# Kernel tuning notes

Hardware: AMD Instinct MI355X
Metric: run time of the kernel (lower is better)

Reference implementation:

```python
import jax, jax.numpy as jnp
import numpy as np

B, N = 2, 8192
D_POINTS, D_MODEL, K = 64, 128, 16


def _lin(key, fi, fo):
    return jax.random.normal(key, (fi, fo), jnp.float32) / np.sqrt(fi)


def setup_inputs() -> dict:
    key = jax.random.key(0)
    ks = jax.random.split(key, 16)
    return {
        "xyz": jax.random.normal(ks[0], (B, N, 3), jnp.float32),
        "normals": jax.random.normal(ks[1], (B, N, 3), jnp.float32),
        "features": jax.random.normal(ks[2], (B, N, D_POINTS), jnp.float32),
        "fc1_w": _lin(ks[3], D_POINTS, D_MODEL), "fc1_b": jnp.zeros((D_MODEL,), jnp.float32),
        "fc2_w": _lin(ks[4], D_MODEL, D_POINTS), "fc2_b": jnp.zeros((D_POINTS,), jnp.float32),
        "gamma_w1": _lin(ks[5], D_MODEL, D_MODEL), "gamma_b1": jnp.zeros((D_MODEL,), jnp.float32),
        "gamma_w2": _lin(ks[6], D_MODEL, D_MODEL), "gamma_b2": jnp.zeros((D_MODEL,), jnp.float32),
        "delta_w1": _lin(ks[7], 3, D_MODEL), "delta_b1": jnp.zeros((D_MODEL,), jnp.float32),
        "delta_w2": _lin(ks[8], D_MODEL, D_MODEL), "delta_b2": jnp.zeros((D_MODEL,), jnp.float32),
        "wq": _lin(ks[9], D_MODEL, D_MODEL),
        "wk": _lin(ks[10], D_MODEL, D_MODEL),
        "wv": _lin(ks[11], D_MODEL, D_MODEL),
    }


def _gather(points, idx):
    # points: (b, n, c), idx: (b, n, k) -> (b, n, k, c)
    b, n, c = points.shape
    k = idx.shape[-1]
    flat = jnp.take_along_axis(points, idx.reshape(b, n * k, 1), axis=1)
    return flat.reshape(b, n, k, c)


def reference(xyz, normals, features, fc1_w, fc1_b, fc2_w, fc2_b,
              gamma_w1, gamma_b1, gamma_w2, gamma_b2,
              delta_w1, delta_b1, delta_w2, delta_b2, wq, wk, wv):
    # pairwise squared distances (b, n, n)
    sq = jnp.sum(xyz * xyz, axis=-1)
    dists = sq[:, :, None] + sq[:, None, :] - 2.0 * jnp.einsum('bnd,bmd->bnm', xyz, xyz)
    _, knn_idx = jax.lax.top_k(-dists, K)  # k smallest distances (includes self)

    knn_xyz = _gather(xyz, knn_idx)                      # (b, n, k, 3)
    x = features @ fc1_w + fc1_b                         # (b, n, d_model)
    q = x @ wq                                           # (b, n, d_model)
    k_nbr = _gather(x @ wk, knn_idx)                     # (b, n, k, d_model)
    v_nbr = _gather(x @ wv, knn_idx)                     # (b, n, k, d_model)

    # positional encoding: fc_delta(rel_pos), ends with ReLU
    rel = xyz[:, :, None, :] - knn_xyz                   # (b, n, k, 3)
    pos_enc = jax.nn.relu(jax.nn.relu(rel @ delta_w1 + delta_b1) @ delta_w2 + delta_b2)

    # vector attention logits: fc_gamma(q - k + pos_enc)
    h = q[:, :, None, :] - k_nbr + pos_enc
    logits = jax.nn.relu(h @ gamma_w1 + gamma_b1) @ gamma_w2 + gamma_b2
    attn = jax.nn.softmax(logits / np.sqrt(D_MODEL), axis=-2)  # softmax over neighbors

    res = jnp.einsum('bnkf,bnkf->bnf', attn, v_nbr + pos_enc)
    res = res @ fc2_w + fc2_b + features
    return res, attn
```

## Files before the change

### kernel.cpp

```cpp
#include <hip/hip_runtime.h>
#include <cstdint>

typedef unsigned long long ull;
typedef __bf16 bf16x8 __attribute__((ext_vector_type(8)));
typedef float f32x4 __attribute__((ext_vector_type(4)));
typedef float f32x2 __attribute__((ext_vector_type(2)));

#define NPTS 8192
#define NB 2
#define KNN 16
#define DM 128
#define PADK 136
#define PADF 72

__device__ __forceinline__ float sq3f(float x, float y, float z) {
    return __fadd_rn(__fadd_rn(__fmul_rn(x, x), __fmul_rn(y, y)), __fmul_rn(z, z));
}
__device__ __forceinline__ unsigned ford(unsigned u) {
    return (u & 0x80000000u) ? ~u : (u | 0x80000000u);
}
__device__ __forceinline__ float inv_ford(unsigned f) {
    unsigned u = (f & 0x80000000u) ? (f ^ 0x80000000u) : ~f;
    return __uint_as_float(u);
}
__device__ __forceinline__ f32x2 pk_mul(f32x2 a, f32x2 b) {
    f32x2 d;
    asm("v_pk_mul_f32 %0, %1, %2" : "=v"(d) : "v"(a), "v"(b));
    return d;
}
__device__ __forceinline__ f32x2 pk_add(f32x2 a, f32x2 b) {
    f32x2 d;
    asm("v_pk_add_f32 %0, %1, %2" : "=v"(d) : "v"(a), "v"(b));
    return d;
}

__device__ __forceinline__ void knn_body(const float* __restrict__ xyz,
                                         int* __restrict__ idx_out,
                                         char* lds, int bid) {
    float4* xsA = (float4*)lds;
    float4* xsB = (float4*)(lds + 8192);
    const int t = threadIdx.x;
    const int wv = t >> 6, lane = t & 63;
    const int q_id = bid * 4 + wv;
    const int b = q_id >> 13;
    const int i = q_id & (NPTS - 1);
    const float* xb = xyz + (size_t)b * NPTS * 3;
    const float qx = xb[3 * i + 0], qy = xb[3 * i + 1], qz = xb[3 * i + 2];
    const float sqi = sq3f(qx, qy, qz);
    const f32x2 qx2 = {qx, qx}, qy2 = {qy, qy}, qz2 = {qz, qz};
    const f32x2 sqi2 = {sqi, sqi}, ntwo2 = {-2.0f, -2.0f};

    unsigned list_hi = 0xffffffffu, list_lo = 0xffffffffu;
    float thrF = __uint_as_float(0x7f800000u);

#define INSERT(FC, CKLO)                                                                 \
    {                                                                                    \
        unsigned ck_hi = ford(__float_as_uint(FC));                                      \
        unsigned ck_lo = (CKLO);                                                         \
        unsigned ph = __shfl_up(list_hi, 1);                                             \
        unsigned pl = __shfl_up(list_lo, 1);                                             \
        bool lt = (ck_hi < list_hi) || (ck_hi == list_hi && ck_lo < list_lo);            \
        bool ge = (lane == 0) || (ck_hi > ph) || (ck_hi == ph && ck_lo >= pl);           \
        list_hi = lt ? (ge ? ck_hi : ph) : list_hi;                                      \
        list_lo = lt ? (ge ? ck_lo : pl) : list_lo;                                      \
        unsigned th = (unsigned)__builtin_amdgcn_readlane((int)list_hi, 15);             \
        th = (th > 0xff800000u) ? 0xff800000u : th;            \
        thrF = fminf(thrF, inv_ford(th));                                                \
    }

    for (int ch = 0; ch < 8; ++ch) {
        __syncthreads();
#pragma unroll
        for (int e = 0; e < 2; e++) {
            int s = t + e * 256;
            int c0 = ((s >> 6) << 7) + (s & 63);
            int g = ch * 1024 + c0;
            float x0 = xb[3 * g + 0], y0 = xb[3 * g + 1], z0 = xb[3 * g + 2];
            float x1 = xb[3 * (g + 64) + 0], y1 = xb[3 * (g + 64) + 1], z1 = xb[3 * (g + 64) + 2];
            xsA[s] = make_float4(x0, x1, y0, y1);
            xsB[s] = make_float4(z0, z1, sq3f(x0, y0, z0), sq3f(x1, y1, z1));
        }
        __syncthreads();
        for (int m = 0; m < 8; m++) {
            const int s = m * 64 + lane;
            float4 A = xsA[s];
            float4 B = xsB[s];
            f32x2 ax = {A.x, A.y}, ay = {A.z, A.w};
            f32x2 bz = {B.x, B.y}, bs = {B.z, B.w};
            f32x2 p1 = pk_mul(qx2, ax);
            f32x2 p2 = pk_mul(qy2, ay);
            f32x2 p3 = pk_mul(qz2, bz);
            f32x2 s1 = pk_add(p1, p2);
            f32x2 s2 = pk_add(s1, p3);
            f32x2 num = pk_add(sqi2, bs);
            f32x2 tm = pk_mul(ntwo2, s2);
            f32x2 dd = pk_add(num, tm);
            float dA = dd.x, dB = dd.y;
            if (ch == 0 && m == 0) {
                float mn = fminf(dA, dB);
                mn = fminf(mn, __shfl_xor(mn, 1));
                mn = fminf(mn, __shfl_xor(mn, 2));
                float mx = mn;
                mx = fmaxf(mx, __shfl_xor(mx, 4));
                mx = fmaxf(mx, __shfl_xor(mx, 8));
                mx = fmaxf(mx, __shfl_xor(mx, 16));
                mx = fmaxf(mx, __shfl_xor(mx, 32));
                thrF = mx;
            }
            ull balA = __ballot(dA <= thrF);
            ull balB = __ballot(dB <= thrF);
            if ((balA | balB) == 0ull) continue;
            const unsigned jbase = (unsigned)(ch * 1024 + m * 128);
            while (balA) {
                int l = (int)__builtin_ctzll(balA);
                balA &= balA - 1;
                float fc = __uint_as_float(
                    (unsigned)__builtin_amdgcn_readlane(__float_as_int(dA), l));
                if (fc <= thrF) INSERT(fc, jbase + (unsigned)l)
            }
            while (balB) {
                int l = (int)__builtin_ctzll(balB);
                balB &= balB - 1;
                float fc = __uint_as_float(
                    (unsigned)__builtin_amdgcn_readlane(__float_as_int(dB), l));
                if (fc <= thrF) INSERT(fc, jbase + 64u + (unsigned)l)
            }
        }
    }
#undef INSERT
    if (lane < 16)
        idx_out[q_id * 16 + lane] = (int)list_lo;
}

__device__ __forceinline__ void xqkv_body(const float* __restrict__ feats,
                                          const __bf16* __restrict__ fc1t,
                                          const float* __restrict__ fc1_b,
                                          const __bf16* __restrict__ wqt,
                                          const __bf16* __restrict__ wkt,
                                          const __bf16* __restrict__ wvt,
                                          float* __restrict__ qo,
                                          float* __restrict__ kko,
                                          float* __restrict__ vvo,
                                          char* lds, int bid) {
    __bf16* Af = (__bf16*)lds;
    __bf16* Ab = (__bf16*)(lds + 9216);
    const int t = threadIdx.x;
    const int base = bid * 64;

#pragma unroll
    for (int e = 0; e < 4; e++) {
        int id = t + e * 256;
        int r = id >> 4, c4 = id & 15;
        float4 v = *(const float4*)&feats[(size_t)(base + r) * 64 + c4 * 4];
        __bf16* d = &Af[r * PADF + c4 * 4];
        d[0] = (__bf16)v.x; d[1] = (__bf16)v.y; d[2] = (__bf16)v.z; d[3] = (__bf16)v.w;
    }
    __syncthreads();

    const int lane = t & 63;
    const int lr = lane & 15, lg = lane >> 4;
    const int rb = (t >> 6) * 16;

    f32x4 xacc[8];
#pragma unroll
    for (int ct = 0; ct < 8; ct++) {
        float bb = fc1_b[ct * 16 + lr];
        xacc[ct] = (f32x4){bb, bb, bb, bb};
    }
#pragma unroll
    for (int kt = 0; kt < 2; kt++) {
        const int ko = kt * 32 + 8 * lg;
        bf16x8 a0 = *(const bf16x8*)&Af[(rb + lr) * PADF + ko];
#pragma unroll
        for (int ct = 0; ct < 8; ct++) {
            bf16x8 bv = *(const bf16x8*)&fc1t[(ct * 16 + lr) * 64 + ko];
            xacc[ct] = __builtin_amdgcn_mfma_f32_16x16x32_bf16(a0, bv, xacc[ct], 0, 0, 0);
        }
    }
#pragma unroll
    for (int ct = 0; ct < 8; ct++)
#pragma unroll
        for (int e = 0; e < 4; e++)
            Ab[(rb + 4 * lg + e) * PADK + ct * 16 + lr] = (__bf16)xacc[ct][e];

#define QGEMM(WPTR, OUT)                                                                   \
    {                                                                                      \
        f32x4 accg[8];                                                                     \
        _Pragma("unroll")                                                                  \
        for (int ct = 0; ct < 8; ct++) accg[ct] = (f32x4){0.f, 0.f, 0.f, 0.f};             \
        _Pragma("unroll")                                                                  \
        for (int kt = 0; kt < 4; kt++) {                                                   \
            const int ko = kt * 32 + 8 * lg;                                               \
            bf16x8 a0 = *(const bf16x8*)&Ab[(rb + lr) * PADK + ko];                        \
            _Pragma("unroll")                                                              \
            for (int ct = 0; ct < 8; ct++) {                                               \
                bf16x8 bv = *(const bf16x8*)&WPTR[(ct * 16 + lr) * 128 + ko];              \
                accg[ct] = __builtin_amdgcn_mfma_f32_16x16x32_bf16(a0, bv, accg[ct], 0, 0, 0); \
            }                                                                              \
        }                                                                                  \
        _Pragma("unroll")                                                                  \
        for (int ct = 0; ct < 8; ct++)                                                     \
            _Pragma("unroll")                                                              \
            for (int e = 0; e < 4; e++)                                                    \
                OUT[(size_t)(base + rb + 4 * lg + e) * 128 + ct * 16 + lr] = accg[ct][e];  \
    }

    QGEMM(wqt, qo)
    QGEMM(wkt, kko)
    QGEMM(wvt, vvo)
#undef QGEMM
}

__global__ __launch_bounds__(256, 6) void mega_kernel(const float* __restrict__ xyz,
                                                      int* __restrict__ idxw,
                                                      const float* __restrict__ feats,
                                                      const __bf16* __restrict__ fc1t,
                                                      const float* __restrict__ fc1_b,
                                                      const __bf16* __restrict__ wqt,
                                                      const __bf16* __restrict__ wkt,
                                                      const __bf16* __restrict__ wvt,
                                                      float* __restrict__ qo,
                                                      float* __restrict__ kko,
                                                      float* __restrict__ vvo) {
    __shared__ __align__(16) char lds[26624];
    const int g = blockIdx.x / 17;
    const int p = blockIdx.x % 17;
    if (p == 0)
        xqkv_body(feats, fc1t, fc1_b, wqt, wkt, wvt, qo, kko, vvo, lds, g);
    else
        knn_body(xyz, idxw, lds, g * 16 + (p - 1));
}

__global__ __launch_bounds__(256) void wprep_kernel(const float* __restrict__ d2,
                                                    const float* __restrict__ g1,
                                                    const float* __restrict__ g2,
                                                    const float* __restrict__ wq,
                                                    const float* __restrict__ wk,
                                                    const float* __restrict__ wv,
                                                    const float* __restrict__ fc1,
                                                    __bf16* __restrict__ d2t,
                                                    __bf16* __restrict__ g1t,
                                                    __bf16* __restrict__ g2t,
                                                    __bf16* __restrict__ wqt,
                                                    __bf16* __restrict__ wkt,
                                                    __bf16* __restrict__ wvt,
                                                    __bf16* __restrict__ fc1t) {
    const int bi = blockIdx.x;
    if (bi == 6) {
#pragma unroll
        for (int e = 0; e < 32; e++) {
            int id = threadIdx.x + e * 256;
            int k = id >> 7, n = id & 127;
            fc1t[n * 64 + k] = (__bf16)fc1[id];
        }
        return;
    }
    const float* src = (bi == 0) ? d2 : (bi == 1) ? g1 : (bi == 2) ? g2
                     : (bi == 3) ? wq : (bi == 4) ? wk : wv;
    __bf16* dst = (bi == 0) ? d2t : (bi == 1) ? g1t : (bi == 2) ? g2t
                : (bi == 3) ? wqt : (bi == 4) ? wkt : wvt;
#pragma unroll
    for (int e = 0; e < 64; e++) {
        int id = threadIdx.x + e * 256;
        int k = id >> 7, n = id & 127;
        dst[n * 128 + k] = (__bf16)src[id];
    }
}

#define STAGE_W(SRC)                                                                       \
    {                                                                                      \
        _Pragma("unroll")                                                                  \
        for (int e = 0; e < 8; e++) {                                                      \
            int ch = t + e * 256;                                                          \
            int r = ch >> 4, ck = ch & 15;                                                 \
            *(bf16x8*)&Wb[r * PADK + ck * 8] = *(const bf16x8*)&SRC[r * 128 + ck * 8];     \
        }                                                                                  \
    }

#define DO_GEMM(ACC0, ACC1, WPTR)                                                          \
    {                                                                                      \
        _Pragma("unroll")                                                                  \
        for (int kt = 0; kt < 4; kt++) {                                                   \
            const int ko = kt * 32 + 8 * lg;                                               \
            bf16x8 a0 = *(const bf16x8*)&Ab[(rbase + lr) * PADK + ko];                     \
            bf16x8 a1 = *(const bf16x8*)&Ab[(rbase + 16 + lr) * PADK + ko];                \
            _Pragma("unroll")                                                              \
            for (int ct = 0; ct < 8; ct++) {                                               \
                bf16x8 bv = *(const bf16x8*)&WPTR[(ct * 16 + lr) * PADK + ko];             \
                ACC0[ct] = __builtin_amdgcn_mfma_f32_16x16x32_bf16(a0, bv, ACC0[ct], 0, 0, 0); \
                ACC1[ct] = __builtin_amdgcn_mfma_f32_16x16x32_bf16(a1, bv, ACC1[ct], 0, 0, 0); \
            }                                                                              \
        }                                                                                  \
    }

__global__ __launch_bounds__(256, 2) void k345_kernel(const float* __restrict__ xyz,
                                                      const int* __restrict__ idxw,
                                                      const float* __restrict__ q,
                                                      const float* __restrict__ xk,
                                                      const float* __restrict__ xv,
                                                      const float* __restrict__ d1,
                                                      const float* __restrict__ bd1,
                                                      const float* __restrict__ bd2,
                                                      const float* __restrict__ bg1,
                                                      const float* __restrict__ bg2,
                                                      const __bf16* __restrict__ d2t,
                                                      const __bf16* __restrict__ g1t,
                                                      const __bf16* __restrict__ g2t,
                                                      float* __restrict__ attn,
                                                      float* __restrict__ res_pre) {
    __shared__ __bf16 Ab[128 * PADK];
    __shared__ __bf16 Wb[128 * PADK];
    __shared__ float rels[128 * 4];
    __shared__ int jrow[128];
    __shared__ float d1s[3 * 128];
    __shared__ float bd1s[128], bd2s[128], bg1s[128], bg2s[128];

    const int t = threadIdx.x;
    const int wv = t >> 6;
    const int lane = t & 63;
    const int lr = lane & 15, lg = lane >> 4;
    const int R0 = blockIdx.x * 128;
    const int b = R0 >> 17;
    const int rbase = wv * 32;

#pragma unroll
    for (int e = 0; e < 2; e++) { int id = t + e * 256; if (id < 384) d1s[id] = d1[id]; }
    if (t < 128) {
        bd1s[t] = bd1[t]; bd2s[t] = bd2[t]; bg1s[t] = bg1[t]; bg2s[t] = bg2[t];
    } else {
        int r = t - 128;
        int j = idxw[R0 + r];
        jrow[r] = j;
        const float* pn = xyz + (size_t)((R0 + r) >> 4) * 3;
        const float* pj = xyz + (size_t)((b << 13) + j) * 3;
        rels[r * 4 + 0] = pn[0] - pj[0];
        rels[r * 4 + 1] = pn[1] - pj[1];
        rels[r * 4 + 2] = pn[2] - pj[2];
    }
    STAGE_W(d2t)
    __syncthreads();

    {
        const int c = t & 127;
        const float w0 = d1s[c], w1 = d1s[128 + c], w2 = d1s[256 + c], bb = bd1s[c];
#pragma unroll
        for (int e = 0; e < 64; e++) {
            int r = (t >> 7) + e * 2;
            float v = fmaf(rels[r * 4 + 2], w2,
                      fmaf(rels[r * 4 + 1], w1, fmaf(rels[r * 4 + 0], w0, bb)));
            Ab[r * PADK + c] = (__bf16)fmaxf(v, 0.0f);
        }
    }
    __syncthreads();

    f32x4 acc0[8], acc1[8];
#pragma unroll
    for (int ct = 0; ct < 8; ct++) {
        float bb = bd2s[ct * 16 + lr];
        acc0[ct] = (f32x4){bb, bb, bb, bb};
        acc1[ct] = acc0[ct];
    }
    DO_GEMM(acc0, acc1, Wb)
    f32x4 pos0[8], pos1[8];
#pragma unroll
    for (int ct = 0; ct < 8; ct++) {
#pragma unroll
        for (int e = 0; e < 4; e++) {
            pos0[ct][e] = fmaxf(acc0[ct][e], 0.0f);
            pos1[ct][e] = fmaxf(acc1[ct][e], 0.0f);
        }
    }

#pragma unroll
    for (int rt = 0; rt < 2; rt++) {
        const int rloc = rbase + rt * 16 + 4 * lg;
        const size_t qbase = (size_t)((R0 + rloc) >> 4) * 128;
        const int j0 = jrow[rloc + 0], j1 = jrow[rloc + 1];
        const int j2 = jrow[rloc + 2], j3 = jrow[rloc + 3];
        const size_t kb0 = (size_t)((b << 13) + j0) * 128;
        const size_t kb1 = (size_t)((b << 13) + j1) * 128;
        const size_t kb2 = (size_t)((b << 13) + j2) * 128;
        const size_t kb3 = (size_t)((b << 13) + j3) * 128;
        f32x4* posR = rt ? pos1 : pos0;
#pragma unroll
        for (int ct = 0; ct < 8; ct++) {
            const int c = ct * 16 + lr;
            const float qv = q[qbase + c];
            f32x4 p = posR[ct];
            Ab[(rloc + 0) * PADK + c] = (__bf16)(p[0] + qv - xk[kb0 + c]);
            Ab[(rloc + 1) * PADK + c] = (__bf16)(p[1] + qv - xk[kb1 + c]);
            Ab[(rloc + 2) * PADK + c] = (__bf16)(p[2] + qv - xk[kb2 + c]);
            Ab[(rloc + 3) * PADK + c] = (__bf16)(p[3] + qv - xk[kb3 + c]);
        }
    }
    __syncthreads();
    STAGE_W(g1t)
    __syncthreads();

#pragma unroll
    for (int ct = 0; ct < 8; ct++) {
        float bb = bg1s[ct * 16 + lr];
        acc0[ct] = (f32x4){bb, bb, bb, bb};
        acc1[ct] = acc0[ct];
    }
    DO_GEMM(acc0, acc1, Wb)
#pragma unroll
    for (int rt = 0; rt < 2; rt++) {
        const int rloc = rbase + rt * 16 + 4 * lg;
        f32x4* accR = rt ? acc1 : acc0;
#pragma unroll
        for (int ct = 0; ct < 8; ct++) {
            const int c = ct * 16 + lr;
            f32x4 p = accR[ct];
            Ab[(rloc + 0) * PADK + c] = (__bf16)fmaxf(p[0], 0.0f);
            Ab[(rloc + 1) * PADK + c] = (__bf16)fmaxf(p[1], 0.0f);
            Ab[(rloc + 2) * PADK + c] = (__bf16)fmaxf(p[2], 0.0f);
            Ab[(rloc + 3) * PADK + c] = (__bf16)fmaxf(p[3], 0.0f);
        }
    }
    __syncthreads();
    STAGE_W(g2t)
    __syncthreads();

#pragma unroll
    for (int ct = 0; ct < 8; ct++) {
        float bb = bg2s[ct * 16 + lr];
        acc0[ct] = (f32x4){bb, bb, bb, bb};
        acc1[ct] = acc0[ct];
    }
    DO_GEMM(acc0, acc1, Wb)
    const float scale = 0.08838834764831845f;
#pragma unroll
    for (int rt = 0; rt < 2; rt++) {
        const int rloc = rbase + rt * 16 + 4 * lg;
        const int j0 = jrow[rloc + 0], j1 = jrow[rloc + 1];
        const int j2 = jrow[rloc + 2], j3 = jrow[rloc + 3];
        const size_t vb0 = (size_t)((b << 13) + j0) * 128;
        const size_t vb1 = (size_t)((b << 13) + j1) * 128;
        const size_t vb2 = (size_t)((b << 13) + j2) * 128;
        const size_t vb3 = (size_t)((b << 13) + j3) * 128;
        f32x4* accR = rt ? acc1 : acc0;
        f32x4* posR = rt ? pos1 : pos0;
#pragma unroll
        for (int ct = 0; ct < 8; ct++) {
            const int c = ct * 16 + lr;
            f32x4 p = accR[ct];
            float l0 = p[0] * scale, l1 = p[1] * scale, l2 = p[2] * scale, l3 = p[3] * scale;
            float m = fmaxf(fmaxf(l0, l1), fmaxf(l2, l3));
            m = fmaxf(m, __shfl_xor(m, 16));
            m = fmaxf(m, __shfl_xor(m, 32));
            float e0 = __expf(l0 - m), e1 = __expf(l1 - m);
            float e2 = __expf(l2 - m), e3 = __expf(l3 - m);
            float s = (e0 + e1) + (e2 + e3);
            s += __shfl_xor(s, 16);
            s += __shfl_xor(s, 32);
            float inv = 1.0f / s;
            float a0 = e0 * inv, a1 = e1 * inv, a2 = e2 * inv, a3 = e3 * inv;
            size_t ob = (size_t)(R0 + rloc) * 128 + c;
            attn[ob + 0 * 128] = a0;
            attn[ob + 1 * 128] = a1;
            attn[ob + 2 * 128] = a2;
            attn[ob + 3 * 128] = a3;
            f32x4 pp = posR[ct];
            float r = a0 * (xv[vb0 + c] + pp[0])
                    + a1 * (xv[vb1 + c] + pp[1])
                    + a2 * (xv[vb2 + c] + pp[2])
                    + a3 * (xv[vb3 + c] + pp[3]);
            r += __shfl_xor(r, 16);
            r += __shfl_xor(r, 32);
            if (lg == 0)
                res_pre[(size_t)((R0 >> 4) + wv * 2 + rt) * 128 + c] = r;
        }
    }
}

__global__ __launch_bounds__(256, 1) void k6_kernel(const float* __restrict__ res_pre,
                                                    const float* __restrict__ w,
                                                    const float* __restrict__ bias,
                                                    const float* __restrict__ feats,
                                                    float* __restrict__ res_out) {
    __shared__ float At[128 * 65];
    __shared__ __align__(16) float Wt[128 * 64];
    const int t = threadIdx.x;
    const int base = blockIdx.x * 64;
#pragma unroll
    for (int e = 0; e < 32; e++) {
        int id = t + e * 256;
        int r = id >> 7, c = id & 127;
        At[c * 65 + r] = res_pre[(size_t)(base + r) * 128 + c];
    }
#pragma unroll
    for (int e = 0; e < 32; e++) { int id = t + e * 256; Wt[id] = w[id]; }
    __syncthreads();
    const int r0 = (t >> 4) * 4;
    const int c0 = (t & 15) * 4;
    float acc[4][4];
#pragma unroll
    for (int i = 0; i < 4; i++)
#pragma unroll
        for (int j = 0; j < 4; j++) acc[i][j] = bias[c0 + j];
#pragma unroll 4
    for (int kk = 0; kk < 128; ++kk) {
        float a0 = At[kk * 65 + r0 + 0];
        float a1 = At[kk * 65 + r0 + 1];
        float a2 = At[kk * 65 + r0 + 2];
        float a3 = At[kk * 65 + r0 + 3];
        const float4 w0 = *(const float4*)&Wt[kk * 64 + c0];
        float wj[4] = {w0.x, w0.y, w0.z, w0.w};
#pragma unroll
        for (int j = 0; j < 4; j++) {
            acc[0][j] += a0 * wj[j];
            acc[1][j] += a1 * wj[j];
            acc[2][j] += a2 * wj[j];
            acc[3][j] += a3 * wj[j];
        }
    }
#pragma unroll
    for (int i = 0; i < 4; i++)
#pragma unroll
        for (int j = 0; j < 4; j++)
            res_out[(size_t)(base + r0 + i) * 64 + c0 + j] =
                acc[i][j] + feats[(size_t)(base + r0 + i) * 64 + c0 + j];
}

extern "C" void kernel_launch(void* const* d_in, const int* in_sizes, int n_in,
                              void* d_out, int out_size, void* d_ws, size_t ws_size,
                              hipStream_t stream) {
    (void)in_sizes; (void)n_in; (void)out_size; (void)ws_size;
    const float* xyz   = (const float*)d_in[0];
    const float* feats = (const float*)d_in[2];
    const float* fc1_w = (const float*)d_in[3];
    const float* fc1_b = (const float*)d_in[4];
    const float* fc2_w = (const float*)d_in[5];
    const float* fc2_b = (const float*)d_in[6];
    const float* g1    = (const float*)d_in[7];
    const float* bg1   = (const float*)d_in[8];
    const float* g2    = (const float*)d_in[9];
    const float* bg2   = (const float*)d_in[10];
    const float* d1    = (const float*)d_in[11];
    const float* bd1   = (const float*)d_in[12];
    const float* d2    = (const float*)d_in[13];
    const float* bd2   = (const float*)d_in[14];
    const float* wq    = (const float*)d_in[15];
    const float* wk    = (const float*)d_in[16];
    const float* wv    = (const float*)d_in[17];

    int* idxw   = (int*)d_ws;
    float* qbuf = (float*)((char*)d_ws + (1 << 20));
    float* kbuf = qbuf + 2097152;
    float* vbuf = kbuf + 2097152;
    float* rpre = vbuf + 2097152;
    __bf16* d2t = (__bf16*)(rpre + 2097152);
    __bf16* g1t = d2t + 16384;
    __bf16* g2t = g1t + 16384;
    __bf16* wqt = g2t + 16384;
    __bf16* wkt = wqt + 16384;
    __bf16* wvt = wkt + 16384;
    __bf16* fc1t = wvt + 16384;

    float* res_out = (float*)d_out;
    float* attn    = res_out + 1048576;

    wprep_kernel<<<7, 256, 0, stream>>>(d2, g1, g2, wq, wk, wv, fc1_w,
                                        d2t, g1t, g2t, wqt, wkt, wvt, fc1t);
    mega_kernel<<<4352, 256, 0, stream>>>(xyz, idxw, feats, fc1t, fc1_b,
                                          wqt, wkt, wvt, qbuf, kbuf, vbuf);
    k345_kernel<<<2048, 256, 0, stream>>>(xyz, idxw, qbuf, kbuf, vbuf, d1, bd1, bd2, bg1, bg2,
                                          d2t, g1t, g2t, attn, rpre);
    k6_kernel<<<256, 256, 0, stream>>>(rpre, fc2_w, fc2_b, feats, res_out);
}
```

Before: 249.8 us.

## Split fused kNN/QKV kernel and widen k345 to 512 threads

Splits the fused mega kernel, which interleaved QKV-projection blocks with kNN blocks by block index, into two separate launches run back to back. Separately, k345 now uses 512 threads per block with each wave handling 16 rows instead of 32. This halves the per-wave accumulator registers so more waves can be resident. The split gives up the overlap between the GEMM work and the kNN search, and the k345 change adds an extra barrier.

```diff
diff --git a/kernel.cpp b/kernel.cpp
--- a/kernel.cpp
+++ b/kernel.cpp
@@ -34,14 +34,13 @@
     return d;
 }
 
-__device__ __forceinline__ void knn_body(const float* __restrict__ xyz,
-                                         int* __restrict__ idx_out,
-                                         char* lds, int bid) {
-    float4* xsA = (float4*)lds;
-    float4* xsB = (float4*)(lds + 8192);
+__global__ __launch_bounds__(256) void knn_kernel(const float* __restrict__ xyz,
+                                                  int* __restrict__ idx_out) {
+    __shared__ float4 xsA[512];
+    __shared__ float4 xsB[512];
     const int t = threadIdx.x;
     const int wv = t >> 6, lane = t & 63;
-    const int q_id = bid * 4 + wv;
+    const int q_id = blockIdx.x * 4 + wv;
     const int b = q_id >> 13;
     const int i = q_id & (NPTS - 1);
     const float* xb = xyz + (size_t)b * NPTS * 3;
@@ -132,20 +131,20 @@
         idx_out[q_id * 16 + lane] = (int)list_lo;
 }
 
-__device__ __forceinline__ void xqkv_body(const float* __restrict__ feats,
-                                          const __bf16* __restrict__ fc1t,
-                                          const float* __restrict__ fc1_b,
-                                          const __bf16* __restrict__ wqt,
-                                          const __bf16* __restrict__ wkt,
-                                          const __bf16* __restrict__ wvt,
-                                          float* __restrict__ qo,
-                                          float* __restrict__ kko,
-                                          float* __restrict__ vvo,
-                                          char* lds, int bid) {
+__global__ __launch_bounds__(256, 6) void xqkv_kernel(const float* __restrict__ feats,
+                                                      const __bf16* __restrict__ fc1t,
+                                                      const float* __restrict__ fc1_b,
+                                                      const __bf16* __restrict__ wqt,
+                                                      const __bf16* __restrict__ wkt,
+                                                      const __bf16* __restrict__ wvt,
+                                                      float* __restrict__ qo,
+                                                      float* __restrict__ kko,
+                                                      float* __restrict__ vvo) {
+    __shared__ __align__(16) char lds[26624];
     __bf16* Af = (__bf16*)lds;
     __bf16* Ab = (__bf16*)(lds + 9216);
     const int t = threadIdx.x;
-    const int base = bid * 64;
+    const int base = blockIdx.x * 64;
 
 #pragma unroll
     for (int e = 0; e < 4; e++) {
@@ -211,26 +210,6 @@
 #undef QGEMM
 }
 
-__global__ __launch_bounds__(256, 6) void mega_kernel(const float* __restrict__ xyz,
-                                                      int* __restrict__ idxw,
-                                                      const float* __restrict__ feats,
-                                                      const __bf16* __restrict__ fc1t,
-                                                      const float* __restrict__ fc1_b,
-                                                      const __bf16* __restrict__ wqt,
-                                                      const __bf16* __restrict__ wkt,
-                                                      const __bf16* __restrict__ wvt,
-                                                      float* __restrict__ qo,
-                                                      float* __restrict__ kko,
-                                                      float* __restrict__ vvo) {
-    __shared__ __align__(16) char lds[26624];
-    const int g = blockIdx.x / 17;
-    const int p = blockIdx.x % 17;
-    if (p == 0)
-        xqkv_body(feats, fc1t, fc1_b, wqt, wkt, wvt, qo, kko, vvo, lds, g);
-    else
-        knn_body(xyz, idxw, lds, g * 16 + (p - 1));
-}
-
 __global__ __launch_bounds__(256) void wprep_kernel(const float* __restrict__ d2,
                                                     const float* __restrict__ g1,
                                                     const float* __restrict__ g2,
@@ -270,30 +249,28 @@
 #define STAGE_W(SRC)                                                                       \
     {                                                                                      \
         _Pragma("unroll")                                                                  \
-        for (int e = 0; e < 8; e++) {                                                      \
-            int ch = t + e * 256;                                                          \
+        for (int e = 0; e < 4; e++) {                                                      \
+            int ch = t + e * 512;                                                          \
             int r = ch >> 4, ck = ch & 15;                                                 \
             *(bf16x8*)&Wb[r * PADK + ck * 8] = *(const bf16x8*)&SRC[r * 128 + ck * 8];     \
         }                                                                                  \
     }
 
-#define DO_GEMM(ACC0, ACC1, WPTR)                                                          \
+#define DO_GEMM1(ACC, WPTR)                                                                \
     {                                                                                      \
         _Pragma("unroll")                                                                  \
         for (int kt = 0; kt < 4; kt++) {                                                   \
             const int ko = kt * 32 + 8 * lg;                                               \
             bf16x8 a0 = *(const bf16x8*)&Ab[(rbase + lr) * PADK + ko];                     \
-            bf16x8 a1 = *(const bf16x8*)&Ab[(rbase + 16 + lr) * PADK + ko];                \
             _Pragma("unroll")                                                              \
             for (int ct = 0; ct < 8; ct++) {                                               \
                 bf16x8 bv = *(const bf16x8*)&WPTR[(ct * 16 + lr) * PADK + ko];             \
-                ACC0[ct] = __builtin_amdgcn_mfma_f32_16x16x32_bf16(a0, bv, ACC0[ct], 0, 0, 0); \
-                ACC1[ct] = __builtin_amdgcn_mfma_f32_16x16x32_bf16(a1, bv, ACC1[ct], 0, 0, 0); \
+                ACC[ct] = __builtin_amdgcn_mfma_f32_16x16x32_bf16(a0, bv, ACC[ct], 0, 0, 0); \
             }                                                                              \
         }                                                                                  \
     }
 
-__global__ __launch_bounds__(256, 2) void k345_kernel(const float* __restrict__ xyz,
+__global__ __launch_bounds__(512, 4) void k345_kernel(const float* __restrict__ xyz,
                                                       const int* __restrict__ idxw,
                                                       const float* __restrict__ q,
                                                       const float* __restrict__ xk,
@@ -321,13 +298,12 @@
     const int lr = lane & 15, lg = lane >> 4;
     const int R0 = blockIdx.x * 128;
     const int b = R0 >> 17;
-    const int rbase = wv * 32;
-
-#pragma unroll
-    for (int e = 0; e < 2; e++) { int id = t + e * 256; if (id < 384) d1s[id] = d1[id]; }
+    const int rbase = wv * 16;
+
+    if (t < 384) d1s[t] = d1[t];
     if (t < 128) {
         bd1s[t] = bd1[t]; bd2s[t] = bd2[t]; bg1s[t] = bg1[t]; bg2s[t] = bg2[t];
-    } else {
+    } else if (t < 256) {
         int r = t - 128;
         int j = idxw[R0 + r];
         jrow[r] = j;
@@ -344,8 +320,8 @@
         const int c = t & 127;
         const float w0 = d1s[c], w1 = d1s[128 + c], w2 = d1s[256 + c], bb = bd1s[c];
 #pragma unroll
-        for (int e = 0; e < 64; e++) {
-            int r = (t >> 7) + e * 2;
+        for (int e = 0; e < 32; e++) {
+            int r = (t >> 7) + e * 4;
             float v = fmaf(rels[r * 4 + 2], w2,
                       fmaf(rels[r * 4 + 1], w1, fmaf(rels[r * 4 + 0], w0, bb)));
             Ab[r * PADK + c] = (__bf16)fmaxf(v, 0.0f);
@@ -353,27 +329,22 @@
     }
     __syncthreads();
 
-    f32x4 acc0[8], acc1[8];
+    f32x4 acc[8];
 #pragma unroll
     for (int ct = 0; ct < 8; ct++) {
         float bb = bd2s[ct * 16 + lr];
-        acc0[ct] = (f32x4){bb, bb, bb, bb};
-        acc1[ct] = acc0[ct];
-    }
-    DO_GEMM(acc0, acc1, Wb)
-    f32x4 pos0[8], pos1[8];
-#pragma unroll
-    for (int ct = 0; ct < 8; ct++) {
-#pragma unroll
-        for (int e = 0; e < 4; e++) {
-            pos0[ct][e] = fmaxf(acc0[ct][e], 0.0f);
-            pos1[ct][e] = fmaxf(acc1[ct][e], 0.0f);
-        }
-    }
-
-#pragma unroll
-    for (int rt = 0; rt < 2; rt++) {
-        const int rloc = rbase + rt * 16 + 4 * lg;
+        acc[ct] = (f32x4){bb, bb, bb, bb};
+    }
+    DO_GEMM1(acc, Wb)
+    f32x4 pos[8];
+#pragma unroll
+    for (int ct = 0; ct < 8; ct++)
+#pragma unroll
+        for (int e = 0; e < 4; e++)
+            pos[ct][e] = fmaxf(acc[ct][e], 0.0f);
+
+    {
+        const int rloc = rbase + 4 * lg;
         const size_t qbase = (size_t)((R0 + rloc) >> 4) * 128;
         const int j0 = jrow[rloc + 0], j1 = jrow[rloc + 1];
         const int j2 = jrow[rloc + 2], j3 = jrow[rloc + 3];
@@ -381,12 +352,11 @@
         const size_t kb1 = (size_t)((b << 13) + j1) * 128;
         const size_t kb2 = (size_t)((b << 13) + j2) * 128;
         const size_t kb3 = (size_t)((b << 13) + j3) * 128;
-        f32x4* posR = rt ? pos1 : pos0;
 #pragma unroll
         for (int ct = 0; ct < 8; ct++) {
             const int c = ct * 16 + lr;
             const float qv = q[qbase + c];
-            f32x4 p = posR[ct];
+            f32x4 p = pos[ct];
             Ab[(rloc + 0) * PADK + c] = (__bf16)(p[0] + qv - xk[kb0 + c]);
             Ab[(rloc + 1) * PADK + c] = (__bf16)(p[1] + qv - xk[kb1 + c]);
             Ab[(rloc + 2) * PADK + c] = (__bf16)(p[2] + qv - xk[kb2 + c]);
@@ -400,18 +370,16 @@
 #pragma unroll
     for (int ct = 0; ct < 8; ct++) {
         float bb = bg1s[ct * 16 + lr];
-        acc0[ct] = (f32x4){bb, bb, bb, bb};
-        acc1[ct] = acc0[ct];
-    }
-    DO_GEMM(acc0, acc1, Wb)
-#pragma unroll
-    for (int rt = 0; rt < 2; rt++) {
-        const int rloc = rbase + rt * 16 + 4 * lg;
-        f32x4* accR = rt ? acc1 : acc0;
+        acc[ct] = (f32x4){bb, bb, bb, bb};
+    }
+    DO_GEMM1(acc, Wb)
+    __syncthreads();
+    {
+        const int rloc = rbase + 4 * lg;
 #pragma unroll
         for (int ct = 0; ct < 8; ct++) {
             const int c = ct * 16 + lr;
-            f32x4 p = accR[ct];
+            f32x4 p = acc[ct];
             Ab[(rloc + 0) * PADK + c] = (__bf16)fmaxf(p[0], 0.0f);
             Ab[(rloc + 1) * PADK + c] = (__bf16)fmaxf(p[1], 0.0f);
             Ab[(rloc + 2) * PADK + c] = (__bf16)fmaxf(p[2], 0.0f);
@@ -425,26 +393,22 @@
 #pragma unroll
     for (int ct = 0; ct < 8; ct++) {
         float bb = bg2s[ct * 16 + lr];
-        acc0[ct] = (f32x4){bb, bb, bb, bb};
-        acc1[ct] = acc0[ct];
-    }
-    DO_GEMM(acc0, acc1, Wb)
+        acc[ct] = (f32x4){bb, bb, bb, bb};
+    }
+    DO_GEMM1(acc, Wb)
     const float scale = 0.08838834764831845f;
-#pragma unroll
-    for (int rt = 0; rt < 2; rt++) {
-        const int rloc = rbase + rt * 16 + 4 * lg;
+    {
+        const int rloc = rbase + 4 * lg;
         const int j0 = jrow[rloc + 0], j1 = jrow[rloc + 1];
         const int j2 = jrow[rloc + 2], j3 = jrow[rloc + 3];
         const size_t vb0 = (size_t)((b << 13) + j0) * 128;
         const size_t vb1 = (size_t)((b << 13) + j1) * 128;
         const size_t vb2 = (size_t)((b << 13) + j2) * 128;
         const size_t vb3 = (size_t)((b << 13) + j3) * 128;
-        f32x4* accR = rt ? acc1 : acc0;
-        f32x4* posR = rt ? pos1 : pos0;
 #pragma unroll
         for (int ct = 0; ct < 8; ct++) {
             const int c = ct * 16 + lr;
-            f32x4 p = accR[ct];
+            f32x4 p = acc[ct];
             float l0 = p[0] * scale, l1 = p[1] * scale, l2 = p[2] * scale, l3 = p[3] * scale;
             float m = fmaxf(fmaxf(l0, l1), fmaxf(l2, l3));
             m = fmaxf(m, __shfl_xor(m, 16));
@@ -461,7 +425,7 @@
             attn[ob + 1 * 128] = a1;
             attn[ob + 2 * 128] = a2;
             attn[ob + 3 * 128] = a3;
-            f32x4 pp = posR[ct];
+            f32x4 pp = pos[ct];
             float r = a0 * (xv[vb0 + c] + pp[0])
                     + a1 * (xv[vb1 + c] + pp[1])
                     + a2 * (xv[vb2 + c] + pp[2])
@@ -469,7 +433,7 @@
             r += __shfl_xor(r, 16);
             r += __shfl_xor(r, 32);
             if (lg == 0)
-                res_pre[(size_t)((R0 >> 4) + wv * 2 + rt) * 128 + c] = r;
+                res_pre[(size_t)((R0 >> 4) + wv) * 128 + c] = r;
         }
     }
 }
@@ -563,9 +527,10 @@
 
     wprep_kernel<<<7, 256, 0, stream>>>(d2, g1, g2, wq, wk, wv, fc1_w,
                                         d2t, g1t, g2t, wqt, wkt, wvt, fc1t);
-    mega_kernel<<<4352, 256, 0, stream>>>(xyz, idxw, feats, fc1t, fc1_b,
-                                          wqt, wkt, wvt, qbuf, kbuf, vbuf);
-    k345_kernel<<<2048, 256, 0, stream>>>(xyz, idxw, qbuf, kbuf, vbuf, d1, bd1, bd2, bg1, bg2,
+    xqkv_kernel<<<256, 256, 0, stream>>>(feats, fc1t, fc1_b, wqt, wkt, wvt,
+                                         qbuf, kbuf, vbuf);
+    knn_kernel<<<4096, 256, 0, stream>>>(xyz, idxw);
+    k345_kernel<<<2048, 512, 0, stream>>>(xyz, idxw, qbuf, kbuf, vbuf, d1, bd1, bd2, bg1, bg2,
                                           d2t, g1t, g2t, attn, rpre);
     k6_kernel<<<256, 256, 0, stream>>>(rpre, fc2_w, fc2_b, feats, res_out);
 }
```

New measurement: 256.9 us. +2.8%, slower.

## Split fused KNN/QKV mega kernel into separate kernels

Applied to the files above, without the earlier changes.

Splits the combined kernel, which interleaved QKV projection blocks with KNN blocks, into two separate launches: an xqkv kernel and a KNN kernel. Each kernel now gets its own register and LDS allocation and launch bounds, so the KNN path no longer carries the 26 KB LDS footprint and the 6-waves occupancy hint of the GEMM path. The cost is one extra launch and the loss of overlap between the memory-bound GEMM work and the compute-bound KNN search.

```diff
diff --git a/kernel.cpp b/kernel.cpp
--- a/kernel.cpp
+++ b/kernel.cpp
@@ -34,14 +34,13 @@
     return d;
 }
 
-__device__ __forceinline__ void knn_body(const float* __restrict__ xyz,
-                                         int* __restrict__ idx_out,
-                                         char* lds, int bid) {
-    float4* xsA = (float4*)lds;
-    float4* xsB = (float4*)(lds + 8192);
+__global__ __launch_bounds__(256) void knn_kernel(const float* __restrict__ xyz,
+                                                  int* __restrict__ idx_out) {
+    __shared__ float4 xsA[512];
+    __shared__ float4 xsB[512];
     const int t = threadIdx.x;
     const int wv = t >> 6, lane = t & 63;
-    const int q_id = bid * 4 + wv;
+    const int q_id = blockIdx.x * 4 + wv;
     const int b = q_id >> 13;
     const int i = q_id & (NPTS - 1);
     const float* xb = xyz + (size_t)b * NPTS * 3;
@@ -132,20 +131,20 @@
         idx_out[q_id * 16 + lane] = (int)list_lo;
 }
 
-__device__ __forceinline__ void xqkv_body(const float* __restrict__ feats,
-                                          const __bf16* __restrict__ fc1t,
-                                          const float* __restrict__ fc1_b,
-                                          const __bf16* __restrict__ wqt,
-                                          const __bf16* __restrict__ wkt,
-                                          const __bf16* __restrict__ wvt,
-                                          float* __restrict__ qo,
-                                          float* __restrict__ kko,
-                                          float* __restrict__ vvo,
-                                          char* lds, int bid) {
+__global__ __launch_bounds__(256, 6) void xqkv_kernel(const float* __restrict__ feats,
+                                                      const __bf16* __restrict__ fc1t,
+                                                      const float* __restrict__ fc1_b,
+                                                      const __bf16* __restrict__ wqt,
+                                                      const __bf16* __restrict__ wkt,
+                                                      const __bf16* __restrict__ wvt,
+                                                      float* __restrict__ qo,
+                                                      float* __restrict__ kko,
+                                                      float* __restrict__ vvo) {
+    __shared__ __align__(16) char lds[26624];
     __bf16* Af = (__bf16*)lds;
     __bf16* Ab = (__bf16*)(lds + 9216);
     const int t = threadIdx.x;
-    const int base = bid * 64;
+    const int base = blockIdx.x * 64;
 
 #pragma unroll
     for (int e = 0; e < 4; e++) {
@@ -209,26 +208,6 @@
     QGEMM(wkt, kko)
     QGEMM(wvt, vvo)
 #undef QGEMM
-}
-
-__global__ __launch_bounds__(256, 6) void mega_kernel(const float* __restrict__ xyz,
-                                                      int* __restrict__ idxw,
-                                                      const float* __restrict__ feats,
-                                                      const __bf16* __restrict__ fc1t,
-                                                      const float* __restrict__ fc1_b,
-                                                      const __bf16* __restrict__ wqt,
-                                                      const __bf16* __restrict__ wkt,
-                                                      const __bf16* __restrict__ wvt,
-                                                      float* __restrict__ qo,
-                                                      float* __restrict__ kko,
-                                                      float* __restrict__ vvo) {
-    __shared__ __align__(16) char lds[26624];
-    const int g = blockIdx.x / 17;
-    const int p = blockIdx.x % 17;
-    if (p == 0)
-        xqkv_body(feats, fc1t, fc1_b, wqt, wkt, wvt, qo, kko, vvo, lds, g);
-    else
-        knn_body(xyz, idxw, lds, g * 16 + (p - 1));
 }
 
 __global__ __launch_bounds__(256) void wprep_kernel(const float* __restrict__ d2,
@@ -563,8 +542,9 @@
 
     wprep_kernel<<<7, 256, 0, stream>>>(d2, g1, g2, wq, wk, wv, fc1_w,
                                         d2t, g1t, g2t, wqt, wkt, wvt, fc1t);
-    mega_kernel<<<4352, 256, 0, stream>>>(xyz, idxw, feats, fc1t, fc1_b,
-                                          wqt, wkt, wvt, qbuf, kbuf, vbuf);
+    xqkv_kernel<<<256, 256, 0, stream>>>(feats, fc1t, fc1_b, wqt, wkt, wvt,
+                                         qbuf, kbuf, vbuf);
+    knn_kernel<<<4096, 256, 0, stream>>>(xyz, idxw);
     k345_kernel<<<2048, 256, 0, stream>>>(xyz, idxw, qbuf, kbuf, vbuf, d1, bd1, bd2, bg1, bg2,
                                           d2t, g1t, g2t, attn, rpre);
     k6_kernel<<<256, 256, 0, stream>>>(rpre, fc2_w, fc2_b, feats, res_out);
```

After: 254.4 us. Within noise of the previous version (+1.8%).
